# Kernel optimization log

Measured on AMD Instinct MI355X. Metric: run time of the kernel, lower is better.

The kernel has to match this reference:

```python
import jax, jax.numpy as jnp
import numpy as np

D_MODEL = 1024
N_HEADS = 16
DK = D_MODEL // N_HEADS


def setup_inputs() -> dict:
    key = jax.random.key(0)
    ks = jax.random.split(key, 5)
    scale = 1.0 / np.sqrt(D_MODEL)
    x = jax.random.normal(ks[0], (2, 2048, D_MODEL), dtype=jnp.float32)
    Wq = jax.random.normal(ks[1], (D_MODEL, D_MODEL), dtype=jnp.float32) * scale
    Wk = jax.random.normal(ks[2], (D_MODEL, D_MODEL), dtype=jnp.float32) * scale
    Wv = jax.random.normal(ks[3], (D_MODEL, D_MODEL), dtype=jnp.float32) * scale
    Wo = jax.random.normal(ks[4], (D_MODEL, D_MODEL), dtype=jnp.float32) * scale
    return {"x": x, "Wq": Wq, "Wk": Wk, "Wv": Wv, "Wo": Wo}


def reference(x, Wq, Wk, Wv, Wo):
    B, S, D = x.shape
    # Projections (nn.Linear applies x @ W.T; weights here are stored as [out, in])
    q = (x @ Wq.T).reshape(B, S, N_HEADS, DK).transpose(0, 2, 1, 3)  # [B,H,S,dk]
    k = (x @ Wk.T).reshape(B, S, N_HEADS, DK).transpose(0, 2, 1, 3)
    v = (x @ Wv.T).reshape(B, S, N_HEADS, DK).transpose(0, 2, 1, 3)
    scores = jnp.einsum("bhqd,bhkd->bhqk", q, k) / jnp.sqrt(jnp.asarray(DK, x.dtype))
    # Note: original's mask branch is a non-in-place masked_fill (no-op); softmax is unmasked.
    attn = jax.nn.softmax(scores, axis=-1)
    out = jnp.einsum("bhqk,bhkd->bhqd", attn, v)  # [B,H,S,dk]
    out = out.transpose(0, 2, 1, 3).reshape(B, S, D)
    return out @ Wo.T
```

## Files before the change

kernel.cpp:

```cpp
#include <hip/hip_runtime.h>
#include <hip/hip_bf16.h>


typedef __attribute__((ext_vector_type(8))) short bf16x8;
typedef __attribute__((ext_vector_type(4))) float f32x4;

#define SEQ     2048

__device__ __forceinline__ unsigned short f2bf(float f) {
    unsigned u = __builtin_bit_cast(unsigned, f);
    u = (u + 0x7FFFu + ((u >> 16) & 1u)) >> 16;
    return (unsigned short)u;
}

__device__ __forceinline__ unsigned pack_bf2(float lo, float hi) {
    return (unsigned)f2bf(lo) | ((unsigned)f2bf(hi) << 16);
}

__device__ __forceinline__ float fexp2(float x) {
    return exp2f(x);
}

__device__ __forceinline__ void gload16(const void* g, void* l) {
    __builtin_amdgcn_global_load_lds(
        (const __attribute__((address_space(1))) unsigned int*)g,
        (__attribute__((address_space(3))) unsigned int*)l, 16, 0, 0);
}

__global__ __launch_bounds__(256) void cast_all(
    const float* __restrict__ x,
    const float* __restrict__ wq, const float* __restrict__ wk,
    const float* __restrict__ wv, const float* __restrict__ wo,
    short* __restrict__ xb,
    short* __restrict__ wqb, short* __restrict__ wkb,
    short* __restrict__ wvb, short* __restrict__ wob)
{
    int bid = blockIdx.x;
    const float* src; short* dst; long base;
    if (bid < 2048) { src = x; dst = xb; base = (long)bid * 2048; }
    else {
        int k = (bid - 2048) >> 9;
        int r = (bid - 2048) & 511;
        base = (long)r * 2048;
        src = (k == 0) ? wq : (k == 1) ? wk : (k == 2) ? wv : wo;
        dst = (k == 0) ? wqb : (k == 1) ? wkb : (k == 2) ? wvb : wob;
    }
    long off = base + (long)threadIdx.x * 8;
    float4 a = *(const float4*)&src[off];
    float4 b = *(const float4*)&src[off + 4];
    union { unsigned short us[8]; uint4 u; } pk;
    pk.us[0] = f2bf(a.x); pk.us[1] = f2bf(a.y); pk.us[2] = f2bf(a.z); pk.us[3] = f2bf(a.w);
    pk.us[4] = f2bf(b.x); pk.us[5] = f2bf(b.y); pk.us[6] = f2bf(b.z); pk.us[7] = f2bf(b.w);
    *(uint4*)&dst[off] = pk.u;
}

__global__ __launch_bounds__(256) void gemm_qkv(
    const short* __restrict__ A,
    const short* __restrict__ W0, const short* __restrict__ W1, const short* __restrict__ W2,
    short* __restrict__ D0, short* __restrict__ D1, short* __restrict__ D2)
{
    __shared__ short At[128 * 32];
    __shared__ short Bt[128 * 32];
    const int tid = threadIdx.x;
    const int w = tid >> 6, l = tid & 63, lg = l >> 4, ln = l & 15;
    const int wr = w >> 1, wc = w & 1;
    const int reg = blockIdx.x >> 3;
    const short* W = (reg == 0) ? W0 : (reg == 1) ? W1 : W2;
    short* Dst     = (reg == 0) ? D0 : (reg == 1) ? D1 : D2;
    const float sc = (reg == 0) ? 0.18033688011112042f : 1.0f;
    const long col0 = (long)(blockIdx.x & 7) * 128;
    const long row0 = (long)blockIdx.y * 128;
    const char* Ab = (const char*)A;
    const char* Wb = (const char*)W;

    f32x4 acc[4][4] = {};

    for (int k0 = 0; k0 < 1024; k0 += 32) {
        __syncthreads();
#pragma unroll
        for (int c = 0; c < 2; ++c) {
            int lin = (c * 4 + w) * 1024 + l * 16;
            int r = lin >> 6, cb = lin & 63;
            gload16(Ab + (size_t)(row0 + r) * 2048 + (size_t)k0 * 2 + cb,
                    (char*)At + (c * 4 + w) * 1024);
            gload16(Wb + (size_t)(col0 + r) * 2048 + (size_t)k0 * 2 + cb,
                    (char*)Bt + (c * 4 + w) * 1024);
        }
        __syncthreads();

        bf16x8 af[4], bfr[4];
#pragma unroll
        for (int i = 0; i < 4; ++i)
            af[i] = *(const bf16x8*)&At[(wr * 64 + i * 16 + ln) * 32 + lg * 8];
#pragma unroll
        for (int j = 0; j < 4; ++j)
            bfr[j] = *(const bf16x8*)&Bt[(wc * 64 + j * 16 + ln) * 32 + lg * 8];
#pragma unroll
        for (int i = 0; i < 4; ++i)
#pragma unroll
            for (int j = 0; j < 4; ++j)
                acc[i][j] = __builtin_amdgcn_mfma_f32_16x16x32_bf16(af[i], bfr[j], acc[i][j], 0, 0, 0);
    }

#pragma unroll
    for (int i = 0; i < 4; ++i)
#pragma unroll
        for (int j = 0; j < 4; ++j)
#pragma unroll
            for (int rr = 0; rr < 4; ++rr) {
                long grow = row0 + wr * 64 + i * 16 + lg * 4 + rr;
                long gcol = col0 + wc * 64 + j * 16 + ln;
                Dst[grow * 1024 + gcol] = (short)f2bf(acc[i][j][rr] * sc);
            }
}

__global__ __launch_bounds__(256) void gemm_bt_f32(
    const short* __restrict__ A, const short* __restrict__ W, float* __restrict__ Cout)
{
    __shared__ short At[128 * 32];
    __shared__ short Bt[128 * 32];
    const int tid = threadIdx.x;
    const int w = tid >> 6, l = tid & 63, lg = l >> 4, ln = l & 15;
    const int wr = w >> 1, wc = w & 1;
    const long row0 = (long)blockIdx.y * 128;
    const long col0 = (long)blockIdx.x * 128;
    const char* Ab = (const char*)A;
    const char* Wb = (const char*)W;

    f32x4 acc[4][4] = {};

    for (int k0 = 0; k0 < 1024; k0 += 32) {
        __syncthreads();
#pragma unroll
        for (int c = 0; c < 2; ++c) {
            int lin = (c * 4 + w) * 1024 + l * 16;
            int r = lin >> 6, cb = lin & 63;
            gload16(Ab + (size_t)(row0 + r) * 2048 + (size_t)k0 * 2 + cb,
                    (char*)At + (c * 4 + w) * 1024);
            gload16(Wb + (size_t)(col0 + r) * 2048 + (size_t)k0 * 2 + cb,
                    (char*)Bt + (c * 4 + w) * 1024);
        }
        __syncthreads();

        bf16x8 af[4], bfr[4];
#pragma unroll
        for (int i = 0; i < 4; ++i)
            af[i] = *(const bf16x8*)&At[(wr * 64 + i * 16 + ln) * 32 + lg * 8];
#pragma unroll
        for (int j = 0; j < 4; ++j)
            bfr[j] = *(const bf16x8*)&Bt[(wc * 64 + j * 16 + ln) * 32 + lg * 8];
#pragma unroll
        for (int i = 0; i < 4; ++i)
#pragma unroll
            for (int j = 0; j < 4; ++j)
                acc[i][j] = __builtin_amdgcn_mfma_f32_16x16x32_bf16(af[i], bfr[j], acc[i][j], 0, 0, 0);
    }

#pragma unroll
    for (int i = 0; i < 4; ++i)
#pragma unroll
        for (int j = 0; j < 4; ++j)
#pragma unroll
            for (int rr = 0; rr < 4; ++rr) {
                long grow = row0 + wr * 64 + i * 16 + lg * 4 + rr;
                long gcol = col0 + wc * 64 + j * 16 + ln;
                Cout[grow * 1024 + gcol] = acc[i][j][rr];
            }
}

__global__ __launch_bounds__(256) void transpose_bf16(
    const short* __restrict__ V, short* __restrict__ VT)
{
    __shared__ short t[64][66];
    const int tid = threadIdx.x;
    const int r = tid >> 2, c4 = (tid & 3) * 16;
    const long m0 = (long)blockIdx.y * 64;
    const long n0 = (long)blockIdx.x * 64;
#pragma unroll
    for (int j = 0; j < 2; ++j) {
        bf16x8 v = *(const bf16x8*)&V[(m0 + r) * 1024 + n0 + c4 + j * 8];
#pragma unroll
        for (int e = 0; e < 8; ++e) t[c4 + j * 8 + e][r] = v[e];
    }
    __syncthreads();
#pragma unroll
    for (int j = 0; j < 2; ++j) {
        bf16x8 v;
#pragma unroll
        for (int e = 0; e < 8; ++e) v[e] = t[r][c4 + j * 8 + e];
        *(bf16x8*)&VT[(n0 + r) * 4096 + m0 + c4 + j * 8] = v;
    }
}

__global__ __launch_bounds__(256) void attn_fwd(
    const short* __restrict__ Q, const short* __restrict__ K,
    const short* __restrict__ VT, short* __restrict__ O)
{
    __shared__ short Kt[64 * 64];
    __shared__ short Vt[64 * 64];
    __shared__ short Pt[4 * 16 * 64];

    const int tid = threadIdx.x;
    const int w = tid >> 6, l = tid & 63, lg = l >> 4, ln = l & 15;
    const int bh = blockIdx.y, b = bh >> 4, h = bh & 15;
    const int qt = blockIdx.x;
    const long qrow0 = (long)b * SEQ + (long)qt * 64;

    bf16x8 qf[2];
#pragma unroll
    for (int kk = 0; kk < 2; ++kk)
        qf[kk] = *(const bf16x8*)&Q[(qrow0 + w * 16 + ln) * 1024 + h * 64 + kk * 32 + lg * 8];

    f32x4 o[4] = {};
    float m_run = -1e30f, l_run = 0.f;

    const char* Kb  = (const char*)K;
    const char* VTb = (const char*)VT;

    for (int t = 0; t < 32; ++t) {
        __syncthreads();
#pragma unroll
        for (int c = 0; c < 2; ++c) {
            int lin = (c * 4 + w) * 1024 + l * 16;
            int r = lin >> 7;
            int cb = (lin & 127) ^ ((r & 7) << 4);
            gload16(Kb + (size_t)(b * SEQ + t * 64 + r) * 2048 + h * 128 + cb,
                    (char*)Kt + (c * 4 + w) * 1024);
            gload16(VTb + (size_t)(h * 64 + r) * 8192 + (size_t)(b * SEQ + t * 64) * 2 + cb,
                    (char*)Vt + (c * 4 + w) * 1024);
        }
        __syncthreads();

        f32x4 s[4] = {};
#pragma unroll
        for (int nb = 0; nb < 4; ++nb) {
            int row = nb * 16 + ln;
#pragma unroll
            for (int kk = 0; kk < 2; ++kk) {
                int cb = (kk * 64 + lg * 16) ^ ((row & 7) << 4);
                bf16x8 kf = *(const bf16x8*)((const char*)Kt + row * 128 + cb);
                s[nb] = __builtin_amdgcn_mfma_f32_16x16x32_bf16(kf, qf[kk], s[nb], 0, 0, 0);
            }
        }

        float mx = s[0][0];
#pragma unroll
        for (int nb = 0; nb < 4; ++nb)
#pragma unroll
            for (int i = 0; i < 4; ++i) mx = fmaxf(mx, s[nb][i]);
        mx = fmaxf(mx, __shfl_xor(mx, 16, 64));
        mx = fmaxf(mx, __shfl_xor(mx, 32, 64));
        float mn = fmaxf(m_run, mx);
        float fac = fexp2(m_run - mn);
        m_run = mn;
        float p[4][4];
        float sum = 0.f;
#pragma unroll
        for (int nb = 0; nb < 4; ++nb)
#pragma unroll
            for (int i = 0; i < 4; ++i) {
                float pv = fexp2(s[nb][i] - mn);
                p[nb][i] = pv;
                sum += pv;
            }
        sum += __shfl_xor(sum, 16, 64);
        sum += __shfl_xor(sum, 32, 64);
        l_run = l_run * fac + sum;

#pragma unroll
        for (int nb = 0; nb < 4; ++nb) {
            unsigned pk0 = pack_bf2(p[nb][0], p[nb][1]);
            unsigned pk1 = pack_bf2(p[nb][2], p[nb][3]);
            int cb = (32 * nb + 8 * lg) ^ ((ln & 7) << 4);
            *(uint2*)((char*)Pt + w * 2048 + ln * 128 + cb) = uint2{ pk0, pk1 };
        }

        float facr[4];
#pragma unroll
        for (int i = 0; i < 4; ++i)
            facr[i] = __shfl(fac, 16 * lg + lg * 4 + i, 64);
#pragma unroll
        for (int nb = 0; nb < 4; ++nb)
#pragma unroll
            for (int i = 0; i < 4; ++i) o[nb][i] *= facr[i];

        bf16x8 pa[2];
#pragma unroll
        for (int kk = 0; kk < 2; ++kk) {
            int cb = (kk * 64 + lg * 16) ^ ((ln & 7) << 4);
            pa[kk] = *(const bf16x8*)((const char*)Pt + w * 2048 + ln * 128 + cb);
        }
#pragma unroll
        for (int nb = 0; nb < 4; ++nb) {
            int row = nb * 16 + ln;
#pragma unroll
            for (int kk = 0; kk < 2; ++kk) {
                int cb = (kk * 64 + lg * 16) ^ ((row & 7) << 4);
                bf16x8 vf = *(const bf16x8*)((const char*)Vt + row * 128 + cb);
                o[nb] = __builtin_amdgcn_mfma_f32_16x16x32_bf16(pa[kk], vf, o[nb], 0, 0, 0);
            }
        }
    }

    float rl[4];
#pragma unroll
    for (int i = 0; i < 4; ++i)
        rl[i] = 1.0f / __shfl(l_run, 16 * lg + lg * 4 + i, 64);
#pragma unroll
    for (int nb = 0; nb < 4; ++nb)
#pragma unroll
        for (int i = 0; i < 4; ++i) {
            float v = o[nb][i] * rl[i];
            O[(qrow0 + w * 16 + lg * 4 + i) * 1024 + h * 64 + nb * 16 + ln] = (short)f2bf(v);
        }
}

extern "C" void kernel_launch(void* const* d_in, const int* in_sizes, int n_in,
                              void* d_out, int out_size, void* d_ws, size_t ws_size,
                              hipStream_t stream)
{
    const float* x  = (const float*)d_in[0];
    const float* wq = (const float*)d_in[1];
    const float* wk = (const float*)d_in[2];
    const float* wv = (const float*)d_in[3];
    const float* wo = (const float*)d_in[4];
    float* out = (float*)d_out;
    char* ws = (char*)d_ws;

    const size_t MB = 1024 * 1024;
    short* Xb  = (short*)(ws);
    short* Wqb = (short*)(ws + 8  * MB);
    short* Wkb = (short*)(ws + 10 * MB);
    short* Wvb = (short*)(ws + 12 * MB);
    short* Wob = (short*)(ws + 14 * MB);
    short* Qb  = (short*)(ws + 16 * MB);
    short* Kb  = (short*)(ws + 24 * MB);
    short* Vb  = (short*)(ws + 32 * MB);
    short* VTb = (short*)(ws + 40 * MB);
    short* Ab  = (short*)(ws + 48 * MB);

    cast_all<<<4096, 256, 0, stream>>>(x, wq, wk, wv, wo, Xb, Wqb, Wkb, Wvb, Wob);

    gemm_qkv<<<dim3(24, 32), 256, 0, stream>>>(Xb, Wqb, Wkb, Wvb, Qb, Kb, Vb);

    transpose_bf16<<<dim3(16, 64), 256, 0, stream>>>(Vb, VTb);

    attn_fwd<<<dim3(32, 32), 256, 0, stream>>>(Qb, Kb, VTb, Ab);

    gemm_bt_f32<<<dim3(8, 32), 256, 0, stream>>>(Ab, Wob, out);
}
```

Before: 232.5 us.

## Split attention over KV halves with merge kernel and lazy rescaling

The attention kernel now splits the key sequence into two halves, one per block, doubling the grid to raise occupancy. Each block writes unnormalized partial outputs plus running max and sum, and a new merge kernel combines them into the final layout. The online softmax also skips rescaling unless the max grows by more than a threshold, and the P tile in shared memory gets a new layout. The costs are an extra launch, the extra partial-output traffic, and bf16 rounding of the unnormalized partials.

```diff
diff --git a/kernel.cpp b/kernel.cpp
--- a/kernel.cpp
+++ b/kernel.cpp
@@ -11,6 +11,10 @@
     unsigned u = __builtin_bit_cast(unsigned, f);
     u = (u + 0x7FFFu + ((u >> 16) & 1u)) >> 16;
     return (unsigned short)u;
+}
+
+__device__ __forceinline__ float bf2f(unsigned short v) {
+    return __builtin_bit_cast(float, ((unsigned)v) << 16);
 }
 
 __device__ __forceinline__ unsigned pack_bf2(float lo, float hi) {
@@ -192,19 +196,24 @@
     }
 }
 
-__global__ __launch_bounds__(256) void attn_fwd(
+__global__ __launch_bounds__(256, 6) void attn_part(
     const short* __restrict__ Q, const short* __restrict__ K,
-    const short* __restrict__ VT, short* __restrict__ O)
+    const short* __restrict__ VT,
+    short* __restrict__ OP0, short* __restrict__ OP1,
+    float2* __restrict__ ML0, float2* __restrict__ ML1)
 {
     __shared__ short Kt[64 * 64];
     __shared__ short Vt[64 * 64];
-    __shared__ short Pt[4 * 16 * 64];
+    __shared__ short Pt[4 * 1024];
 
     const int tid = threadIdx.x;
     const int w = tid >> 6, l = tid & 63, lg = l >> 4, ln = l & 15;
     const int bh = blockIdx.y, b = bh >> 4, h = bh & 15;
-    const int qt = blockIdx.x;
+    const int qt = blockIdx.x >> 1, half = blockIdx.x & 1;
     const long qrow0 = (long)b * SEQ + (long)qt * 64;
+
+    short*  __restrict__ OPh = half ? OP1 : OP0;
+    float2* __restrict__ MLh = half ? ML1 : ML0;
 
     bf16x8 qf[2];
 #pragma unroll
@@ -217,7 +226,10 @@
     const char* Kb  = (const char*)K;
     const char* VTb = (const char*)VT;
 
-    for (int t = 0; t < 32; ++t) {
+    char*       Pw = (char*)Pt + w * 2048 + l * 8;
+    const char* Pr = (char*)Pt + w * 2048 + (lg >> 1) * 512 + (lg & 1) * 256 + ln * 8;
+
+    for (int t = half * 16; t < half * 16 + 16; ++t) {
         __syncthreads();
 #pragma unroll
         for (int c = 0; c < 2; ++c) {
@@ -250,45 +262,49 @@
             for (int i = 0; i < 4; ++i) mx = fmaxf(mx, s[nb][i]);
         mx = fmaxf(mx, __shfl_xor(mx, 16, 64));
         mx = fmaxf(mx, __shfl_xor(mx, 32, 64));
-        float mn = fmaxf(m_run, mx);
-        float fac = fexp2(m_run - mn);
-        m_run = mn;
+
+        if (__any(mx > m_run + 8.0f)) {
+            float mn = fmaxf(m_run, mx);
+            float fac = fexp2(m_run - mn);
+            m_run = mn;
+            l_run *= fac;
+            float facr[4];
+#pragma unroll
+            for (int i = 0; i < 4; ++i)
+                facr[i] = __shfl(fac, 16 * lg + lg * 4 + i, 64);
+#pragma unroll
+            for (int nb = 0; nb < 4; ++nb)
+#pragma unroll
+                for (int i = 0; i < 4; ++i) o[nb][i] *= facr[i];
+        }
+
         float p[4][4];
         float sum = 0.f;
 #pragma unroll
         for (int nb = 0; nb < 4; ++nb)
 #pragma unroll
             for (int i = 0; i < 4; ++i) {
-                float pv = fexp2(s[nb][i] - mn);
+                float pv = fexp2(s[nb][i] - m_run);
                 p[nb][i] = pv;
                 sum += pv;
             }
         sum += __shfl_xor(sum, 16, 64);
         sum += __shfl_xor(sum, 32, 64);
-        l_run = l_run * fac + sum;
+        l_run += sum;
 
 #pragma unroll
         for (int nb = 0; nb < 4; ++nb) {
-            unsigned pk0 = pack_bf2(p[nb][0], p[nb][1]);
-            unsigned pk1 = pack_bf2(p[nb][2], p[nb][3]);
-            int cb = (32 * nb + 8 * lg) ^ ((ln & 7) << 4);
-            *(uint2*)((char*)Pt + w * 2048 + ln * 128 + cb) = uint2{ pk0, pk1 };
-        }
-
-        float facr[4];
-#pragma unroll
-        for (int i = 0; i < 4; ++i)
-            facr[i] = __shfl(fac, 16 * lg + lg * 4 + i, 64);
-#pragma unroll
-        for (int nb = 0; nb < 4; ++nb)
-#pragma unroll
-            for (int i = 0; i < 4; ++i) o[nb][i] *= facr[i];
+            uint2 pw = { pack_bf2(p[nb][0], p[nb][1]), pack_bf2(p[nb][2], p[nb][3]) };
+            *(uint2*)(Pw + nb * 512) = pw;
+        }
 
         bf16x8 pa[2];
 #pragma unroll
         for (int kk = 0; kk < 2; ++kk) {
-            int cb = (kk * 64 + lg * 16) ^ ((ln & 7) << 4);
-            pa[kk] = *(const bf16x8*)((const char*)Pt + w * 2048 + ln * 128 + cb);
+            uint2 d0 = *(const uint2*)(Pr + kk * 1024);
+            uint2 d1 = *(const uint2*)(Pr + kk * 1024 + 128);
+            uint4 u4 = { d0.x, d0.y, d1.x, d1.y };
+            pa[kk] = __builtin_bit_cast(bf16x8, u4);
         }
 #pragma unroll
         for (int nb = 0; nb < 4; ++nb) {
@@ -302,17 +318,41 @@
         }
     }
 
-    float rl[4];
-#pragma unroll
-    for (int i = 0; i < 4; ++i)
-        rl[i] = 1.0f / __shfl(l_run, 16 * lg + lg * 4 + i, 64);
+    const long Rbase = (long)bh * SEQ + qt * 64 + w * 16;
 #pragma unroll
     for (int nb = 0; nb < 4; ++nb)
 #pragma unroll
         for (int i = 0; i < 4; ++i) {
-            float v = o[nb][i] * rl[i];
-            O[(qrow0 + w * 16 + lg * 4 + i) * 1024 + h * 64 + nb * 16 + ln] = (short)f2bf(v);
-        }
+            long R = Rbase + lg * 4 + i;
+            OPh[R * 64 + nb * 16 + ln] = (short)f2bf(o[nb][i]);
+        }
+    if (lg == 0)
+        MLh[Rbase + ln] = float2{ m_run, l_run };
+}
+
+__global__ __launch_bounds__(256) void attn_merge(
+    const short* __restrict__ O0, const short* __restrict__ O1,
+    const float2* __restrict__ ML0, const float2* __restrict__ ML1,
+    short* __restrict__ Ab)
+{
+    int gid = blockIdx.x * 256 + threadIdx.x;
+    int R = gid >> 3, d0 = (gid & 7) * 8;
+    float2 a = ML0[R];
+    float2 c = ML1[R];
+    float M = fmaxf(a.x, c.x);
+    float w0 = fexp2(a.x - M), w1 = fexp2(c.x - M);
+    float rden = 1.0f / (w0 * a.y + w1 * c.y);
+    bf16x8 v0 = *(const bf16x8*)&O0[(long)R * 64 + d0];
+    bf16x8 v1 = *(const bf16x8*)&O1[(long)R * 64 + d0];
+    int bh = R >> 11, s = R & 2047, b = bh >> 4, h = bh & 15;
+    union { unsigned short us[8]; uint4 u; } pk;
+#pragma unroll
+    for (int e = 0; e < 8; ++e) {
+        float f0 = bf2f((unsigned short)v0[e]);
+        float f1 = bf2f((unsigned short)v1[e]);
+        pk.us[e] = f2bf((w0 * f0 + w1 * f1) * rden);
+    }
+    *(uint4*)&Ab[((long)(b * 2048 + s)) * 1024 + h * 64 + d0] = pk.u;
 }
 
 extern "C" void kernel_launch(void* const* d_in, const int* in_sizes, int n_in,
@@ -338,6 +378,10 @@
     short* Vb  = (short*)(ws + 32 * MB);
     short* VTb = (short*)(ws + 40 * MB);
     short* Ab  = (short*)(ws + 48 * MB);
+    short*  OP0 = (short*)(ws);
+    float2* ML0 = (float2*)(ws + 8 * MB);
+    float2* ML1 = (float2*)(ws + 8 * MB + 512 * 1024);
+    short*  OP1 = (short*)(ws + 32 * MB);
 
     cast_all<<<4096, 256, 0, stream>>>(x, wq, wk, wv, wo, Xb, Wqb, Wkb, Wvb, Wob);
 
@@ -345,7 +389,9 @@
 
     transpose_bf16<<<dim3(16, 64), 256, 0, stream>>>(Vb, VTb);
 
-    attn_fwd<<<dim3(32, 32), 256, 0, stream>>>(Qb, Kb, VTb, Ab);
+    attn_part<<<dim3(64, 32), 256, 0, stream>>>(Qb, Kb, VTb, OP0, OP1, ML0, ML1);
+
+    attn_merge<<<2048, 256, 0, stream>>>(OP0, OP1, ML0, ML1, Ab);
 
     gemm_bt_f32<<<dim3(8, 32), 256, 0, stream>>>(Ab, Wob, out);
 }
```

Result: faster. 222.5 us (-4.3%).
